# Kernel tuning notes

Hardware: AMD Instinct MI355X
Metric: run time of the kernel (lower is better)

## Reference

```python
import jax, jax.numpy as jnp
import numpy as np

N = 50000
L = 16            # number of topological levels
PER = N // L      # nodes per level
DEG = 16          # in-degree for non-source nodes
D = 64            # feature dim


def setup_inputs() -> dict:
    key = jax.random.key(0)
    k1, k2, k3 = jax.random.split(key, 3)
    feat = jax.random.normal(k1, (N, D), dtype=jnp.float32)
    delay = jax.random.uniform(k2, (N, D), dtype=jnp.float32)
    intra_delay = jax.random.uniform(k3, (N, D), dtype=jnp.float32)

    # Build a layered DAG: node i has level i // PER; every node with level >= 1
    # receives DEG edges from uniformly random nodes in strictly earlier levels.
    rng = np.random.default_rng(0)
    dst_np = np.repeat(np.arange(PER, N), DEG)               # [E]
    level_start = (dst_np // PER) * PER                      # first node of dst's level
    src_np = np.floor(rng.random(dst_np.shape) * level_start).astype(np.int64)
    node_levels_np = (np.arange(N) // PER).astype(np.int32)

    return {
        "feat": feat,
        "delay": delay,
        "intra_delay": intra_delay,
        "src": jnp.asarray(src_np, dtype=jnp.int32),
        "dst": jnp.asarray(dst_np, dtype=jnp.int32),
        "node_levels": jnp.asarray(node_levels_np, dtype=jnp.int32),
    }


def reference(feat, delay, intra_delay, src, dst, node_levels):
    # Topological propagation (flag_distance=True path):
    #   for each level l = 1..L-1:
    #     m_e        = feat[src_e] + intra_delay[src_e]      (message)
    #     agg_v      = max over incoming edges of m_e        (fn.max reduce)
    #     feat_v     = agg_v + delay_v   for v in level l    (apply node func)
    n = feat.shape[0]
    for l in range(1, L):
        msg = feat[src] + intra_delay[src]                       # [E, D]
        agg = jax.ops.segment_max(msg, dst, num_segments=n)      # [N, D]
        updated = agg + delay                                    # [N, D]
        mask = (node_levels == l)[:, None]                       # [N, 1]
        feat = jnp.where(mask, updated, feat)
    return feat
```

## Files before the change

kernel.cpp:

```cpp
#include <hip/hip_runtime.h>
#include <hip/hip_bf16.h>


#define NN    50000
#define LVL   16
#define PER   3125
#define DEG   16
#define DF    64

__global__ void __launch_bounds__(256) prop_level(
    float* __restrict__ feat,
    const float* __restrict__ intra,
    const float* __restrict__ delay,
    const int*  __restrict__ src,
    int level_start)
{
    const int idx = blockIdx.x * 4 + (threadIdx.x >> 6);
    if (idx >= PER) return;
    const int v = level_start + idx;
    const int d = threadIdx.x & 63;
    const long ebase = (long)(v - PER) * DEG;

    float m = -INFINITY;
#pragma unroll
    for (int k = 0; k < DEG; ++k) {
        const int s = src[ebase + k];
        const float val = feat[(long)s * DF + d] + intra[(long)s * DF + d];
        m = fmaxf(m, val);
    }
    feat[(long)v * DF + d] = m + delay[(long)v * DF + d];
}

extern "C" void kernel_launch(void* const* d_in, const int* in_sizes, int n_in,
                              void* d_out, int out_size, void* d_ws, size_t ws_size,
                              hipStream_t stream) {
    const float* feat  = (const float*)d_in[0];
    const float* delay = (const float*)d_in[1];
    const float* intra = (const float*)d_in[2];
    const int*   src   = (const int*)d_in[3];
    float* out = (float*)d_out;

    hipMemcpyAsync(out, feat, (size_t)NN * DF * sizeof(float),
                   hipMemcpyDeviceToDevice, stream);

    const int blocks = (PER + 3) / 4;
    for (int l = 1; l < LVL; ++l) {
        prop_level<<<blocks, 256, 0, stream>>>(out, intra, delay, src, l * PER);
    }
}
```

Baseline: 83.42 us.

## Fuse all levels into one persistent kernel with grid barriers and precomputed messages

Replaces the 15 per-level launches and the full device-to-device copy with a single persistent kernel of 256 blocks that crosses levels through an atomic-counter grid barrier. It keeps a message buffer holding feat+intra per node, so each gather reads one array instead of two. Only level 0 is copied up front, and each later level is written as it is produced. This removes launch gaps and half of the gather traffic, but adds barrier spin cost, a workspace dependency, and relies on all 256 blocks being co-resident.

```diff
diff --git a/kernel.cpp b/kernel.cpp
--- a/kernel.cpp
+++ b/kernel.cpp
@@ -8,25 +8,75 @@
 #define DEG   16
 #define DF    64
 
+#define NBLK  256
+#define NTHR  256
+#define NWAVES ((NBLK * NTHR) / 64)
+
+__device__ __forceinline__ void grid_barrier(unsigned* counter, unsigned target) {
+    __syncthreads();
+    if (threadIdx.x == 0) {
+        __hip_atomic_fetch_add(counter, 1u, __ATOMIC_RELEASE, __HIP_MEMORY_SCOPE_AGENT);
+        while (__hip_atomic_load(counter, __ATOMIC_RELAXED, __HIP_MEMORY_SCOPE_AGENT) < target) {
+            __builtin_amdgcn_s_sleep(1);
+        }
+        __builtin_amdgcn_fence(__ATOMIC_ACQUIRE, "agent");
+    }
+    __syncthreads();
+}
+
+__global__ void __launch_bounds__(NTHR) prop_all(
+    const float* __restrict__ feat,
+    const float* __restrict__ delay,
+    const float* __restrict__ intra,
+    const int*  __restrict__ src,
+    float* __restrict__ out,
+    float* __restrict__ msg,
+    unsigned* __restrict__ counter)
+{
+    const int tid = blockIdx.x * NTHR + threadIdx.x;
+
+    for (int i = tid; i < PER * DF; i += NBLK * NTHR) {
+        const float f = feat[i];
+        out[i] = f;
+        msg[i] = f + intra[i];
+    }
+
+    const int wid = tid >> 6;
+    const int d   = threadIdx.x & 63;
+
+    for (int l = 1; l < LVL; ++l) {
+        grid_barrier(counter, (unsigned)(l * NBLK));
+        for (int idx = wid; idx < PER; idx += NWAVES) {
+            const int v = __builtin_amdgcn_readfirstlane(l * PER + idx);
+            const int* sp = src + (size_t)(v - PER) * DEG;
+            float m = -INFINITY;
+#pragma unroll
+            for (int k = 0; k < DEG; ++k) {
+                const int s = sp[k];
+                m = fmaxf(m, msg[(size_t)s * DF + d]);
+            }
+            const float o = m + delay[(size_t)v * DF + d];
+            out[(size_t)v * DF + d] = o;
+            if (l < LVL - 1)
+                msg[(size_t)v * DF + d] = o + intra[(size_t)v * DF + d];
+        }
+    }
+}
+
 __global__ void __launch_bounds__(256) prop_level(
-    float* __restrict__ feat,
-    const float* __restrict__ intra,
-    const float* __restrict__ delay,
-    const int*  __restrict__ src,
-    int level_start)
+    float* __restrict__ feat, const float* __restrict__ intra,
+    const float* __restrict__ delay, const int* __restrict__ src, int level_start)
 {
     const int idx = blockIdx.x * 4 + (threadIdx.x >> 6);
     if (idx >= PER) return;
     const int v = level_start + idx;
     const int d = threadIdx.x & 63;
     const long ebase = (long)(v - PER) * DEG;
-
     float m = -INFINITY;
 #pragma unroll
     for (int k = 0; k < DEG; ++k) {
         const int s = src[ebase + k];
-        const float val = feat[(long)s * DF + d] + intra[(long)s * DF + d];
-        m = fmaxf(m, val);
+        m = fmaxf(m, feat[(long)s * DF + d] + intra[(long)s * DF + d]);
     }
     feat[(long)v * DF + d] = m + delay[(long)v * DF + d];
 }
@@ -40,11 +90,17 @@
     const int*   src   = (const int*)d_in[3];
     float* out = (float*)d_out;
 
-    hipMemcpyAsync(out, feat, (size_t)NN * DF * sizeof(float),
-                   hipMemcpyDeviceToDevice, stream);
-
-    const int blocks = (PER + 3) / 4;
-    for (int l = 1; l < LVL; ++l) {
-        prop_level<<<blocks, 256, 0, stream>>>(out, intra, delay, src, l * PER);
+    const size_t need = 256 + (size_t)NN * DF * sizeof(float);
+    if (ws_size >= need) {
+        unsigned* counter = (unsigned*)d_ws;
+        float*    msg     = (float*)((char*)d_ws + 256);
+        hipMemsetAsync(d_ws, 0, 256, stream);
+        prop_all<<<NBLK, NTHR, 0, stream>>>(feat, delay, intra, src, out, msg, counter);
+    } else {
+        hipMemcpyAsync(out, feat, (size_t)NN * DF * sizeof(float),
+                       hipMemcpyDeviceToDevice, stream);
+        const int blocks = (PER + 3) / 4;
+        for (int l = 1; l < LVL; ++l)
+            prop_level<<<blocks, 256, 0, stream>>>(out, intra, delay, src, l * PER);
     }
 }
```

After: 294.1 us. 3.53x slower.

## Fuse all levels into one persistent kernel with per-chunk software barriers

Applied to the files above, without the earlier changes.

Replaces the fifteen per-level launches with one persistent kernel of 256 blocks. The feature dimension is split into 8 chunks of 8 floats, and each group of 32 blocks owns one chunk and synchronises only within its group through atomic counters in workspace. Messages (feat+intra) and delay+intra are precomputed into a chunk-transposed layout, so each level does a single gather-max per edge, and the output is recovered at the end by subtracting intra. This is meant to remove launch overhead and halve gather traffic. In exchange it needs a large workspace, relies on all 256 blocks being co-resident for the spin barriers, and adds extra full-array passes plus a subtraction that can introduce rounding differences.

```diff
diff --git a/kernel.cpp b/kernel.cpp
--- a/kernel.cpp
+++ b/kernel.cpp
@@ -8,25 +8,127 @@
 #define DEG   16
 #define DF    64
 
+#define NBLK  256
+#define NTHR  1024
+#define NCH   8
+#define BPC   (NBLK / NCH)
+#define NUNIT ((PER + 7) / 8)
+
+#define OFF_CCNT 0
+#define OFF_CREL 1024
+#define OFF_GCNT 2048
+#define OFF_GREL 2176
+#define OFF_MSGT 4096
+#define MSGT_BYTES ((size_t)NN * DF * 4)
+#define OFF_DITT (4096 + MSGT_BYTES)
+#define WS_NEED  (OFF_DITT + MSGT_BYTES)
+
+__device__ __forceinline__ void st_sc1_f(float* p, float v) {
+    __hip_atomic_store(p, v, __ATOMIC_RELAXED, __HIP_MEMORY_SCOPE_AGENT);
+}
+__device__ __forceinline__ void st_sc1_u(unsigned* p, unsigned v) {
+    __hip_atomic_store(p, v, __ATOMIC_RELAXED, __HIP_MEMORY_SCOPE_AGENT);
+}
+__device__ __forceinline__ unsigned ld_sc1_u(const unsigned* p) {
+    return __hip_atomic_load(p, __ATOMIC_RELAXED, __HIP_MEMORY_SCOPE_AGENT);
+}
+
+__device__ __forceinline__ void sw_barrier(unsigned* cnt, unsigned* rel,
+                                           unsigned phase, unsigned nb,
+                                           bool leader) {
+    asm volatile("s_barrier" ::: "memory");
+    if (threadIdx.x == 0) {
+        __hip_atomic_fetch_add(cnt, 1u, __ATOMIC_RELAXED,
+                               __HIP_MEMORY_SCOPE_AGENT);
+        if (leader) {
+            while (ld_sc1_u(cnt) < phase * nb) __builtin_amdgcn_s_sleep(1);
+            st_sc1_u(rel, phase);
+        } else {
+            while (ld_sc1_u(rel) < phase) __builtin_amdgcn_s_sleep(1);
+        }
+    }
+    asm volatile("s_barrier" ::: "memory");
+}
+
+__global__ void __launch_bounds__(NTHR) prop_chunked(
+    const float* __restrict__ feat,
+    const float* __restrict__ delay,
+    const float* __restrict__ intra,
+    const int*  __restrict__ src,
+    float* __restrict__ out,
+    char*  __restrict__ ws)
+{
+    float*    msgT = (float*)(ws + OFF_MSGT);
+    float*    ditT = (float*)(ws + OFF_DITT);
+    unsigned* ccnt = (unsigned*)(ws + OFF_CCNT);
+    unsigned* crel = (unsigned*)(ws + OFF_CREL);
+    unsigned* gcnt = (unsigned*)(ws + OFF_GCNT);
+    unsigned* grel = (unsigned*)(ws + OFF_GREL);
+
+    const int b   = blockIdx.x;
+    const int c   = b & 7;
+    const int tid = b * NTHR + threadIdx.x;
+
+    for (int i = tid; i < NN * DF; i += NBLK * NTHR) {
+        const int v = i >> 6, d = i & 63;
+        const int tix = ((d >> 3) * NN + v) * 8 + (d & 7);
+        const float itv = intra[i];
+        if (v < PER) st_sc1_f(&msgT[tix], feat[i] + itv);
+        else         st_sc1_f(&ditT[tix], delay[i] + itv);
+    }
+    asm volatile("s_waitcnt vmcnt(0)" ::: "memory");
+    sw_barrier(gcnt, grel, 1u, NBLK, b == 0);
+
+    const int u     = (b >> 3) * 16 + (threadIdx.x >> 6);
+    const int lane  = threadIdx.x & 63;
+    const int n     = lane >> 3, j = lane & 7;
+    const int nv    = u * 8 + n;
+    const bool act  = (nv < PER);
+    const int cbase = c * NN;
+    unsigned* mycnt = ccnt + c * 32;
+    unsigned* myrel = crel + c * 32;
+    const bool lead = (b == c);
+
+    for (int l = 1; l < LVL; ++l) {
+        if (act) {
+            const int v  = l * PER + nv;
+            const int eb = (v - PER) * DEG;
+            float m = -INFINITY;
+#pragma unroll
+            for (int k = 0; k < DEG; ++k) {
+                const int s = src[eb + k];
+                m = fmaxf(m, msgT[(cbase + s) * 8 + j]);
+            }
+            st_sc1_f(&msgT[(cbase + v) * 8 + j],
+                     m + ditT[(cbase + v) * 8 + j]);
+        }
+        asm volatile("s_waitcnt vmcnt(0)" ::: "memory");
+        if (l < LVL - 1)
+            sw_barrier(mycnt, myrel, (unsigned)l, BPC, lead);
+    }
+    sw_barrier(gcnt, grel, 2u, NBLK, b == 0);
+
+    for (int i = tid; i < NN * DF; i += NBLK * NTHR) {
+        const int v = i >> 6, d = i & 63;
+        if (v < PER) out[i] = feat[i];
+        else         out[i] = msgT[((d >> 3) * NN + v) * 8 + (d & 7)] - intra[i];
+    }
+}
+
 __global__ void __launch_bounds__(256) prop_level(
-    float* __restrict__ feat,
-    const float* __restrict__ intra,
-    const float* __restrict__ delay,
-    const int*  __restrict__ src,
-    int level_start)
+    float* __restrict__ feat, const float* __restrict__ intra,
+    const float* __restrict__ delay, const int* __restrict__ src, int level_start)
 {
     const int idx = blockIdx.x * 4 + (threadIdx.x >> 6);
     if (idx >= PER) return;
     const int v = level_start + idx;
     const int d = threadIdx.x & 63;
     const long ebase = (long)(v - PER) * DEG;
-
     float m = -INFINITY;
 #pragma unroll
     for (int k = 0; k < DEG; ++k) {
         const int s = src[ebase + k];
-        const float val = feat[(long)s * DF + d] + intra[(long)s * DF + d];
-        m = fmaxf(m, val);
+        m = fmaxf(m, feat[(long)s * DF + d] + intra[(long)s * DF + d]);
     }
     feat[(long)v * DF + d] = m + delay[(long)v * DF + d];
 }
@@ -40,11 +142,15 @@
     const int*   src   = (const int*)d_in[3];
     float* out = (float*)d_out;
 
-    hipMemcpyAsync(out, feat, (size_t)NN * DF * sizeof(float),
-                   hipMemcpyDeviceToDevice, stream);
-
-    const int blocks = (PER + 3) / 4;
-    for (int l = 1; l < LVL; ++l) {
-        prop_level<<<blocks, 256, 0, stream>>>(out, intra, delay, src, l * PER);
+    if (ws_size >= WS_NEED) {
+        hipMemsetAsync(d_ws, 0, 4096, stream);
+        prop_chunked<<<NBLK, NTHR, 0, stream>>>(feat, delay, intra, src, out,
+                                                (char*)d_ws);
+    } else {
+        hipMemcpyAsync(out, feat, (size_t)NN * DF * sizeof(float),
+                       hipMemcpyDeviceToDevice, stream);
+        const int blocks = (PER + 3) / 4;
+        for (int l = 1; l < LVL; ++l)
+            prop_level<<<blocks, 256, 0, stream>>>(out, intra, delay, src, l * PER);
     }
 }
```

After: 95.58 us. 1.15x slower.

## Fuse all levels into one persistent kernel with per-channel-chunk software barriers

Applied to the files above, without the earlier changes.

Replaces the fifteen per-level launches with a single persistent kernel of 256 blocks. The blocks are split into 8 feature-chunk groups, and each group synchronises through its own global-memory barrier. Each node's message (feat+intra) is precomputed into a chunk-transposed workspace, so gathers read 8 contiguous floats and skip one load and an add per edge. The next level's delay and intra are prefetched before each barrier, and only level 0 of the output is copied instead of the whole array. This targets launch overhead and gather traffic, but it relies on all 256 large blocks being co-resident for the spin barriers and needs a workspace large enough to hold the message table.

```diff
diff --git a/kernel.cpp b/kernel.cpp
--- a/kernel.cpp
+++ b/kernel.cpp
@@ -8,25 +8,140 @@
 #define DEG   16
 #define DF    64
 
+#define NBLK  256
+#define NTHR  1024
+#define NCH   8
+#define BPC   32
+
+#define OFF_SLOTS 0
+#define OFF_REL   4096
+#define OFF_MSGT  8192
+#define MSGT_BYTES ((size_t)NN * DF * 4)
+#define WS_NEED   (OFF_MSGT + MSGT_BYTES)
+
+__device__ __forceinline__ void st_sc1_f(float* p, float v) {
+    __hip_atomic_store(p, v, __ATOMIC_RELAXED, __HIP_MEMORY_SCOPE_AGENT);
+}
+__device__ __forceinline__ void st_sc1_u(unsigned* p, unsigned v) {
+    __hip_atomic_store(p, v, __ATOMIC_RELAXED, __HIP_MEMORY_SCOPE_AGENT);
+}
+__device__ __forceinline__ unsigned ld_sc1_u(const unsigned* p) {
+    return __hip_atomic_load(p, __ATOMIC_RELAXED, __HIP_MEMORY_SCOPE_AGENT);
+}
+
+__device__ __forceinline__ void chunk_barrier(unsigned* slots, unsigned* rel,
+                                              int rank, unsigned phase) {
+    asm volatile("s_barrier" ::: "memory");
+    const int w    = threadIdx.x >> 6;
+    const int lane = threadIdx.x & 63;
+    if (rank == 0) {
+        if (w == 0) {
+            if (lane == 0) st_sc1_u(&slots[0], phase);
+            for (;;) {
+                const unsigned v = (lane < BPC) ? ld_sc1_u(&slots[lane]) : phase;
+                if (__all(v >= phase)) break;
+                __builtin_amdgcn_s_sleep(1);
+            }
+            if (lane == 0) st_sc1_u(rel, phase);
+        }
+    } else if (threadIdx.x == 0) {
+        st_sc1_u(&slots[rank], phase);
+        while (ld_sc1_u(rel) < phase) __builtin_amdgcn_s_sleep(1);
+    }
+    asm volatile("s_barrier" ::: "memory");
+}
+
+__global__ void __launch_bounds__(NTHR) prop_chunk2(
+    const float* __restrict__ feat,
+    const float* __restrict__ delay,
+    const float* __restrict__ intra,
+    const int*  __restrict__ src,
+    float* __restrict__ out,
+    char*  __restrict__ ws)
+{
+    float* msgT = (float*)(ws + OFF_MSGT);
+    const int b     = blockIdx.x;
+    const int c     = b & 7;
+    const int rank  = b >> 3;
+    unsigned* slots = (unsigned*)(ws + OFF_SLOTS) + c * 64;
+    unsigned* rel   = (unsigned*)(ws + OFF_REL)  + c * 32;
+    const int cbase = c * NN;
+
+    {
+        const int i = rank * NTHR + threadIdx.x;
+        if (i < PER * 8) {
+            const int v = i >> 3, jj = i & 7;
+            const int dd = c * 8 + jj;
+            st_sc1_f(&msgT[(size_t)(cbase + v) * 8 + jj],
+                     feat[(size_t)v * DF + dd] + intra[(size_t)v * DF + dd]);
+        }
+    }
+
+    const int w    = threadIdx.x >> 6;
+    const int lane = threadIdx.x & 63;
+    const int n    = lane >> 3, j = lane & 7;
+    const int u    = rank * 16 + w;
+    const int nv   = u * 8 + n;
+    const bool act = (nv < PER);
+    const int d    = c * 8 + j;
+
+    float dl = 0.f, it = 0.f;
+    if (act) {
+        const int v1 = PER + nv;
+        dl = delay[(size_t)v1 * DF + d];
+        it = intra[(size_t)v1 * DF + d];
+        int warm = src[(size_t)(v1 - PER) * DEG + 2 * j];
+        asm volatile("" :: "v"(warm));
+    }
+
+    asm volatile("s_waitcnt vmcnt(0)" ::: "memory");
+    chunk_barrier(slots, rel, rank, 1u);
+
+    for (int l = 1; l < LVL; ++l) {
+        float dln = 0.f, itn = 0.f;
+        if (act) {
+            const int v = l * PER + nv;
+            const size_t eb = (size_t)(v - PER) * DEG;
+            float m = -INFINITY;
+#pragma unroll
+            for (int k = 0; k < DEG; ++k) {
+                const int s = src[eb + k];
+                m = fmaxf(m, msgT[(size_t)(cbase + s) * 8 + j]);
+            }
+            const float o = m + dl;
+            st_sc1_f(&out[(size_t)v * DF + d], o);
+            if (l < LVL - 1)
+                st_sc1_f(&msgT[(size_t)(cbase + v) * 8 + j], o + it);
+            if (l + 1 < LVL) {
+                const int vn = (l + 1) * PER + nv;
+                dln = delay[(size_t)vn * DF + d];
+                itn = intra[(size_t)vn * DF + d];
+                int warm = src[(size_t)(vn - PER) * DEG + 2 * j];
+                asm volatile("" :: "v"(warm));
+            }
+        }
+        dl = dln; it = itn;
+        if (l < LVL - 1) {
+            asm volatile("s_waitcnt vmcnt(0)" ::: "memory");
+            chunk_barrier(slots, rel, rank, (unsigned)(l + 1));
+        }
+    }
+}
+
 __global__ void __launch_bounds__(256) prop_level(
-    float* __restrict__ feat,
-    const float* __restrict__ intra,
-    const float* __restrict__ delay,
-    const int*  __restrict__ src,
-    int level_start)
+    float* __restrict__ feat, const float* __restrict__ intra,
+    const float* __restrict__ delay, const int* __restrict__ src, int level_start)
 {
     const int idx = blockIdx.x * 4 + (threadIdx.x >> 6);
     if (idx >= PER) return;
     const int v = level_start + idx;
     const int d = threadIdx.x & 63;
     const long ebase = (long)(v - PER) * DEG;
-
     float m = -INFINITY;
 #pragma unroll
     for (int k = 0; k < DEG; ++k) {
         const int s = src[ebase + k];
-        const float val = feat[(long)s * DF + d] + intra[(long)s * DF + d];
-        m = fmaxf(m, val);
+        m = fmaxf(m, feat[(long)s * DF + d] + intra[(long)s * DF + d]);
     }
     feat[(long)v * DF + d] = m + delay[(long)v * DF + d];
 }
@@ -40,11 +155,17 @@
     const int*   src   = (const int*)d_in[3];
     float* out = (float*)d_out;
 
-    hipMemcpyAsync(out, feat, (size_t)NN * DF * sizeof(float),
-                   hipMemcpyDeviceToDevice, stream);
-
-    const int blocks = (PER + 3) / 4;
-    for (int l = 1; l < LVL; ++l) {
-        prop_level<<<blocks, 256, 0, stream>>>(out, intra, delay, src, l * PER);
+    if (ws_size >= WS_NEED) {
+        hipMemsetAsync(d_ws, 0, 8192, stream);
+        hipMemcpyAsync(out, feat, (size_t)PER * DF * sizeof(float),
+                       hipMemcpyDeviceToDevice, stream);
+        prop_chunk2<<<NBLK, NTHR, 0, stream>>>(feat, delay, intra, src, out,
+                                               (char*)d_ws);
+    } else {
+        hipMemcpyAsync(out, feat, (size_t)NN * DF * sizeof(float),
+                       hipMemcpyDeviceToDevice, stream);
+        const int blocks = (PER + 3) / 4;
+        for (int l = 1; l < LVL; ++l)
+            prop_level<<<blocks, 256, 0, stream>>>(out, intra, delay, src, l * PER);
     }
 }
```

Result: slower. 92.35 us (+10.7%).
